# Optimization experiments

Measured on AMD Instinct MI355X. Metric: run time of the kernel, lower is better.

The kernel has to match this reference:

```python
import jax, jax.numpy as jnp
import numpy as np

DIM = 384
HEADS = 12
K = 3          # kernel_size
PAD = 1
STRIDE = 1
B, H, W = 8, 56, 56


def conv1x1(x, w, b=None):
    # x: [B,C,H,W], w: [O,C]
    y = jnp.einsum('bchw,oc->bohw', x, w)
    if b is not None:
        y = y + b[None, :, None, None]
    return y


def unfold(x, k, p, s):
    # torch nn.Unfold: returns patches [B, C, k*k, nH, nW], kernel row-major, channel-major overall
    Bx, C, Hx, Wx = x.shape
    nH = (Hx + 2 * p - k) // s + 1
    nW = (Wx + 2 * p - k) // s + 1
    xp = jnp.pad(x, ((0, 0), (0, 0), (p, p), (p, p)))
    cols = [xp[:, :, i:i + s * nH:s, j:j + s * nW:s] for i in range(k) for j in range(k)]
    return jnp.stack(cols, axis=2), nH, nW


def fold(col, Hx, Wx, k, p, s):
    # torch F.fold (col2im): scatter-add overlapping windows. col: [B, C, k*k, nH, nW]
    Bx, C, _, nH, nW = col.shape
    canvas = jnp.zeros((Bx, C, Hx + 2 * p, Wx + 2 * p), col.dtype)
    idx = 0
    for i in range(k):
        for j in range(k):
            canvas = canvas.at[:, :, i:i + s * nH:s, j:j + s * nW:s].add(col[:, :, idx])
            idx += 1
    return canvas[:, :, p:p + Hx, p:p + Wx]


def setup_inputs() -> dict:
    key = jax.random.key(0)
    ks = jax.random.split(key, 5)
    k2 = K * K
    x = jax.random.normal(ks[0], (B, DIM, H, W), dtype=jnp.float32)
    v_w = jax.random.normal(ks[1], (DIM, DIM), dtype=jnp.float32) * 0.02
    v_b = jnp.zeros((DIM,), dtype=jnp.float32)
    attn_w = jax.random.normal(ks[2], (k2 * k2 * HEADS, DIM), dtype=jnp.float32) * 0.02
    proj_w = jax.random.normal(ks[3], (DIM, DIM), dtype=jnp.float32) * 0.02
    return {'x': x, 'v_w': v_w, 'v_b': v_b, 'attn_w': attn_w, 'proj_w': proj_w}


def reference(x, v_w, v_b, attn_w, proj_w):
    Bx, C, Hx, Wx = x.shape
    k2 = K * K
    hd = C // HEADS  # head dim
    # value projection + unfold into overlapping k x k windows
    v = conv1x1(x, v_w, v_b)
    vcol, nH, nW = unfold(v, K, PAD, STRIDE)        # [B, C, k2, nH, nW]
    L = nH * nW
    v = vcol.reshape(Bx, HEADS, hd, k2, L)          # split C = (heads, hd), heads slow
    v = v.transpose(0, 1, 4, 3, 2)                  # [B, n, L, k2(d), hd]
    # adaptive avg pool to (nH, nW); with stride=1 this is identity (pool window 1)
    ph, pw = Hx // nH, Wx // nW
    xp = x.reshape(Bx, C, nH, ph, nW, pw).mean(axis=(3, 5))
    # per-pixel attention logits, channel layout = ((i*k2 + d)*HEADS + head)
    a = jnp.einsum('bchw,oc->bohw', xp, attn_w)     # [B, k2*k2*n, nH, nW]
    a = a.reshape(Bx, k2, k2, HEADS, L)             # [B, i, d, n, L]
    a = a.transpose(0, 3, 4, 1, 2)                  # [B, n, L, i, d]
    a = jax.nn.softmax(a, axis=-1)
    out = jnp.einsum('bnlid,bnldh->bnlih', a, v)    # [B, n, L, i, hd]
    out = out.transpose(0, 1, 4, 3, 2)              # [B, n, hd, i, L] -> channel (n*hd+h)
    out = out.reshape(Bx, C, k2, nH, nW)
    out = fold(out, Hx, Wx, K, PAD, STRIDE)         # scatter-add windows back
    return conv1x1(out, proj_w)
```

## Files before the change

### kernel.cpp

```cpp
#include <hip/hip_runtime.h>
#include <hip/hip_bf16.h>

#define DIM   384
#define HEADS 12
#define K2    9
#define HH    56
#define WW    56
#define HWP   3136
#define BB    8
#define AO    972
#define AOP   976
#define MCAT  1408
#define PP    3200
#define PPAD  3600
#define W60   60

#define WBLK     2688
#define HALOBLK  696

typedef __hip_bfloat16 bf16;
typedef short bf16x8 __attribute__((ext_vector_type(8)));
typedef short bf16x4v __attribute__((ext_vector_type(4)));
typedef float f32x4 __attribute__((ext_vector_type(4)));
typedef float f32x2 __attribute__((ext_vector_type(2)));

static __device__ __forceinline__ float b2f(bf16 v) { return __bfloat162float(v); }
static __device__ __forceinline__ float bs2f(short s) {
    return __uint_as_float(((unsigned int)(unsigned short)s) << 16);
}
static __device__ __forceinline__ short f2bs(float f) {
    __hip_bfloat16 h = __float2bfloat16(f);
    return *(short*)&h;
}
static __device__ __forceinline__ f32x2 unpk(unsigned int u) {
    f32x2 r;
    r[0] = __uint_as_float(u << 16);
    r[1] = __uint_as_float(u & 0xffff0000u);
    return r;
}

static __device__ __forceinline__ void gl_lds16(const bf16* g, bf16* l) {
    __builtin_amdgcn_global_load_lds(
        (const __attribute__((address_space(1))) unsigned int*)g,
        (__attribute__((address_space(3))) unsigned int*)l, 16, 0, 0);
}

__global__ __launch_bounds__(256) void prep_kernel(
        const float* __restrict__ x, const float* __restrict__ v_w,
        const float* __restrict__ attn_w, const float* __restrict__ proj_w,
        bf16* __restrict__ xT, bf16* __restrict__ wcat, bf16* __restrict__ wp,
        bf16* __restrict__ vP) {
    const int bid = blockIdx.x;
    if (bid < 400) {
        const int lane = threadIdx.x & 63, w = threadIdx.x >> 6;
        const int p = (bid % 50) * 64 + lane;
        const int b = bid / 50;
        bf16* dst = xT + ((size_t)b * PP + p) * DIM;
        if (p >= HWP) {
            bf16x8 z = {};
            for (int cg = w; cg < 48; cg += 4) *(bf16x8*)(dst + cg * 8) = z;
            return;
        }
        const float* src = x + (size_t)b * DIM * HWP + p;
        for (int cg = w; cg < 48; cg += 4) {
            bf16x8 v;
#pragma unroll
            for (int j = 0; j < 8; j++) v[j] = f2bs(src[(size_t)(cg * 8 + j) * HWP]);
            *(bf16x8*)(dst + cg * 8) = v;
        }
    } else if (bid < 400 + WBLK) {
        const int idx = (bid - 400) * 256 + threadIdx.x;
        const int NCAT = MCAT * DIM;
        if (idx < NCAT) {
            const int row = idx / DIM, col = idx % DIM;
            float v;
            if (row < 384) v = v_w[row * DIM + col];
            else { const int r2 = row - 384; v = (r2 < AO) ? attn_w[r2 * DIM + col] : 0.f; }
            *(short*)&wcat[idx] = f2bs(v);
        } else {
            const int j = idx - NCAT;
            if (j < 384 * DIM) *(short*)&wp[j] = f2bs(proj_w[j]);
        }
    } else {
        const int hidx = (bid - 400 - WBLK) * 256 + threadIdx.x;
        const int b = hidx / 22272;
        const int r = hidx % 22272;
        const int hp = r / 48, cgi = r % 48;
        int row, col;
        if (hp < 240) {
            const int rr = hp / 60;
            row = (rr < 2) ? rr : rr + 56;
            col = hp % 60;
        } else {
            const int h2 = hp - 240;
            row = 2 + (h2 >> 2);
            const int c4 = h2 & 3;
            col = (c4 < 2) ? c4 : c4 + 56;
        }
        bf16x8 z = {};
        *(bf16x8*)(vP + ((size_t)b * PPAD + row * W60 + col) * DIM + cgi * 8) = z;
    }
}

#define GEMM_MAIN_LOOP_V4(Ab, Bb, lA, lB, acc)                                 \
    for (int k0 = 0; k0 < DIM; k0 += 64) {                                     \
        _Pragma("unroll")                                                      \
        for (int r = 0; r < 4; r++) {                                          \
            int idx = r * 256 + t;                                             \
            int row = idx >> 3;                                                \
            int kq = ((idx & 7) - (row >> 1)) & 7;                             \
            gl_lds16(Ab + (size_t)row * DIM + k0 + kq * 8, lA + idx * 8);      \
        }                                                                      \
        _Pragma("unroll")                                                      \
        for (int r = 0; r < 4; r++) {                                          \
            int idx = r * 256 + t;                                             \
            int row = idx >> 3;                                                \
            int kq = ((idx & 7) - (row >> 1)) & 7;                             \
            gl_lds16(Bb + (size_t)row * DIM + k0 + kq * 8, lB + idx * 8);      \
        }                                                                      \
        __syncthreads();                                                       \
        _Pragma("unroll")                                                      \
        for (int h = 0; h < 2; h++) {                                          \
            const int swzh = (((h << 2) + quad + (l16 >> 1)) & 7) * 8;         \
            bf16x8 af[4], bfr[4];                                              \
            _Pragma("unroll")                                                  \
            for (int mt = 0; mt < 4; mt++)                                     \
                af[mt] = *(const bf16x8*)(lA + (wm * 64 + mt * 16 + l16) * 64 + swzh); \
            _Pragma("unroll")                                                  \
            for (int nt = 0; nt < 4; nt++)                                     \
                bfr[nt] = *(const bf16x8*)(lB + (wn * 64 + nt * 16 + l16) * 64 + swzh); \
            _Pragma("unroll")                                                  \
            for (int mt = 0; mt < 4; mt++)                                     \
                _Pragma("unroll")                                              \
                for (int nt = 0; nt < 4; nt++)                                 \
                    acc[mt][nt] = __builtin_amdgcn_mfma_f32_16x16x32_bf16(     \
                        af[mt], bfr[nt], acc[mt][nt], 0, 0, 0);                \
        }                                                                      \
        __syncthreads();                                                       \
    }

__global__ __launch_bounds__(256) void gemm12_kernel(
        const bf16* __restrict__ A, const bf16* __restrict__ Bt,
        const float* __restrict__ bias, bf16* __restrict__ vP,
        bf16* __restrict__ lT) {
    __shared__ bf16 lds[16384];
    bf16* lA = lds;
    bf16* lB = lds + 8192;
    const int t = threadIdx.x;
    const int lane = t & 63, w = t >> 6;
    const int wm = w & 1, wn = w >> 1;
    const int quad = lane >> 4, l16 = lane & 15;

    const int bid = blockIdx.x;
    const int swz = (bid & 7) * 275 + (bid >> 3);
    const int mtile = swz % 11;
    const int nb = swz / 11;
    const int ntile = nb % 25;
    const int b = nb / 25;
    const int n0 = ntile * 128;
    const int m0 = mtile * 128;

    const bf16* Ab = A + (size_t)m0 * DIM;
    const bf16* Bb = Bt + ((size_t)b * PP + n0) * DIM;

    f32x4 acc[4][4] = {};
    GEMM_MAIN_LOOP_V4(Ab, Bb, lA, lB, acc)

    const bool isv = (m0 < 384);
    const int ch0 = isv ? m0 : m0 - 384;

    bf16* wbuf = lds + w * 1152;
    const int nr = lane >> 2;
    const int mc = (lane & 3) * 16;
#pragma unroll
    for (int nt = 0; nt < 4; nt++) {
#pragma unroll
        for (int mt = 0; mt < 4; mt++) {
            float4 bi = make_float4(0.f, 0.f, 0.f, 0.f);
            if (isv) bi = *(const float4*)(bias + ch0 + wm * 64 + mt * 16 + quad * 4);
            bf16x4v pk;
            pk[0] = f2bs(acc[mt][nt][0] + bi.x);
            pk[1] = f2bs(acc[mt][nt][1] + bi.y);
            pk[2] = f2bs(acc[mt][nt][2] + bi.z);
            pk[3] = f2bs(acc[mt][nt][3] + bi.w);
            *(bf16x4v*)(wbuf + l16 * 72 + mt * 16 + quad * 4) = pk;
        }
        bf16x8 v0 = *(const bf16x8*)(wbuf + nr * 72 + mc);
        bf16x8 v1 = *(const bf16x8*)(wbuf + nr * 72 + mc + 8);
        const int p = n0 + wn * 64 + nt * 16 + nr;
        const int cc = ch0 + wm * 64 + mc;
        if (p < HWP && (isv || cc < AOP)) {
            bf16* dp;
            if (isv) {
                const int y = p / WW;
                dp = vP + ((size_t)b * PPAD + p + y * 4 + 122) * DIM + cc;
            } else {
                dp = lT + ((size_t)b * PP + p) * AOP + cc;
            }
            *(bf16x8*)dp = v0;
            *(bf16x8*)(dp + 8) = v1;
        }
    }
}

__global__ __launch_bounds__(256) void gemm_planar_kernel(
        const bf16* __restrict__ A, const bf16* __restrict__ Bt,
        float* __restrict__ out) {
    __shared__ bf16 lds[16384];
    bf16* lA = lds;
    bf16* lB = lds + 8192;
    const int t = threadIdx.x;
    const int lane = t & 63, w = t >> 6;
    const int wm = w & 1, wn = w >> 1;
    const int quad = lane >> 4, l16 = lane & 15;

    const int bid = blockIdx.x;
    const int swz = (bid & 7) * 75 + (bid >> 3);
    const int mtile = swz % 3;
    const int nb = swz / 3;
    const int ntile = nb % 25;
    const int b = nb / 25;
    const int n0 = ntile * 128;
    const int m0 = mtile * 128;

    const bf16* Ab = A + (size_t)m0 * DIM;
    const bf16* Bb = Bt + ((size_t)b * PP + n0) * DIM;

    f32x4 acc[4][4] = {};
    GEMM_MAIN_LOOP_V4(Ab, Bb, lA, lB, acc)

#pragma unroll
    for (int mt = 0; mt < 4; mt++) {
#pragma unroll
        for (int nt = 0; nt < 4; nt++) {
            int p = n0 + wn * 64 + nt * 16 + l16;
            if (p >= HWP) continue;
#pragma unroll
            for (int reg = 0; reg < 4; reg++) {
                int o = m0 + wm * 64 + mt * 16 + quad * 4 + reg;
                out[((size_t)b * DIM + o) * HWP + p] = acc[mt][nt][reg];
            }
        }
    }
}

__global__ __launch_bounds__(384) void attn_fold_kernel(
        const bf16* __restrict__ lT, const bf16* __restrict__ vP,
        bf16* __restrict__ cT) {
    __shared__ bf16 P[8 * 9 * 12 * 9];
    __shared__ float Wf[8 * 25 * 12];
    const int t = threadIdx.x;
    const int b = blockIdx.x & 7;
    const int pix0 = (blockIdx.x >> 3) * 8;
    const int Y = pix0 / WW, X0 = pix0 % WW;

    for (int r = t; r < 864; r += 384) {
        const int px = r / 108, rem = r % 108;
        const int i = rem / 12, n = rem % 12;
        const int ir = i / 3, ic = i % 3;
        const int yi = Y + 1 - ir, xi = X0 + px + 1 - ic;
        bf16* Pd = &P[r * 9];
        if (yi < 0 || yi >= HH || xi < 0 || xi >= WW) {
#pragma unroll
            for (int d = 0; d < K2; d++) *(short*)&Pd[d] = 0;
        } else {
            const bf16* base = lT + ((size_t)b * PP + yi * WW + xi) * AOP + i * 108 + n;
            float lv[K2];
            float m = -1e30f;
#pragma unroll
            for (int d = 0; d < K2; d++) {
                lv[d] = b2f(base[d * 12]);
                m = fmaxf(m, lv[d]);
            }
            float s = 0.f;
#pragma unroll
            for (int d = 0; d < K2; d++) { lv[d] = __expf(lv[d] - m); s += lv[d]; }
            const float inv = 1.f / s;
#pragma unroll
            for (int d = 0; d < K2; d++) *(short*)&Pd[d] = f2bs(lv[d] * inv);
        }
    }
    __syncthreads();

    if (t < 300) {
        const int off = t / 12, n = t % 12;
        const int dy = off / 5 - 2, dx = off % 5 - 2;
        const int ir_lo = max(0, -dy), ir_hi = min(2, 2 - dy);
        const int ic_lo = max(0, -dx), ic_hi = min(2, 2 - dx);
#pragma unroll
        for (int px = 0; px < 8; px++) {
            float wsum = 0.f;
            for (int ir = ir_lo; ir <= ir_hi; ir++)
                for (int ic = ic_lo; ic <= ic_hi; ic++) {
                    const int i = ir * 3 + ic;
                    const int d = (dy + ir) * 3 + (dx + ic);
                    wsum += b2f(P[((px * 9 + i) * 12 + n) * 9 + d]);
                }
            Wf[(px * 25 + off) * 12 + n] = wsum;
        }
    }
    __syncthreads();

    const int px = t / 48, cg = t % 48;
    const int X = X0 + px;
    const int n = cg >> 2;
    const float* Wp = &Wf[px * 300 + n];
    const bf16* vbp = vP + ((size_t)b * PPAD + (size_t)(Y + 2) * W60 + (X + 2)) * DIM + cg * 8;
    f32x2 a2[4] = {};
#pragma unroll
    for (int dy = -2; dy <= 2; dy++) {
        const bf16* rowb = vbp + dy * (W60 * DIM);
        const float* wrow = Wp + (dy + 2) * 60;
#pragma unroll
        for (int dx = -2; dx <= 2; dx++) {
            const float w = wrow[(dx + 2) * 12];
            const uint4 d = *(const uint4*)(rowb + dx * DIM);
            f32x2 w2; w2[0] = w; w2[1] = w;
            a2[0] = __builtin_elementwise_fma(unpk(d.x), w2, a2[0]);
            a2[1] = __builtin_elementwise_fma(unpk(d.y), w2, a2[1]);
            a2[2] = __builtin_elementwise_fma(unpk(d.z), w2, a2[2]);
            a2[3] = __builtin_elementwise_fma(unpk(d.w), w2, a2[3]);
        }
    }
    bf16x8 po;
#pragma unroll
    for (int j = 0; j < 4; j++) {
        po[2 * j]     = f2bs(a2[j][0]);
        po[2 * j + 1] = f2bs(a2[j][1]);
    }
    *(bf16x8*)(cT + ((size_t)b * PP + pix0 + px) * DIM + cg * 8) = po;
}

extern "C" void kernel_launch(void* const* d_in, const int* in_sizes, int n_in,
                              void* d_out, int out_size, void* d_ws, size_t ws_size,
                              hipStream_t stream) {
    const float* x      = (const float*)d_in[0];
    const float* v_w    = (const float*)d_in[1];
    const float* v_b    = (const float*)d_in[2];
    const float* attn_w = (const float*)d_in[3];
    const float* proj_w = (const float*)d_in[4];
    float* out = (float*)d_out;

    bf16* xT    = (bf16*)d_ws;
    bf16* vP    = xT + (size_t)BB * PP * DIM;
    bf16* lT    = vP + (size_t)BB * PPAD * DIM;
    bf16* wcat  = lT + (size_t)BB * PP * AOP;
    bf16* wp    = wcat + (size_t)MCAT * DIM;
    bf16* cT    = xT;

    const int nprep = 400 + WBLK + HALOBLK;
    prep_kernel<<<nprep, 256, 0, stream>>>(x, v_w, attn_w, proj_w, xT, wcat, wp, vP);

    gemm12_kernel<<<2200, 256, 0, stream>>>(wcat, xT, v_b, vP, lT);
    attn_fold_kernel<<<3136, 384, 0, stream>>>(lT, vP, cT);
    gemm_planar_kernel<<<600, 256, 0, stream>>>(wp, cT, out);
}
```

Baseline: 204.7 us.

## Double-buffer LDS in GEMM main loop and raise priority around MFMA compute

Splits the GEMM K-loop into separate stage and compute macros and uses two LDS buffers per operand. The next K-slice's global-to-LDS loads are issued before the MFMA work on the current slice, which halves the barriers per slice and overlaps load latency with compute. s_setprio is raised around the MFMA section. LDS use doubles to 64 KB per block, which may reduce how many blocks fit on a CU.

```diff
diff --git a/kernel.cpp b/kernel.cpp
--- a/kernel.cpp
+++ b/kernel.cpp
@@ -102,40 +102,56 @@
     }
 }
 
-#define GEMM_MAIN_LOOP_V4(Ab, Bb, lA, lB, acc)                                 \
-    for (int k0 = 0; k0 < DIM; k0 += 64) {                                     \
+#define GEMM_STAGE(Ab, Bb, lA, lB, koff)                                       \
+    {                                                                          \
         _Pragma("unroll")                                                      \
         for (int r = 0; r < 4; r++) {                                          \
             int idx = r * 256 + t;                                             \
             int row = idx >> 3;                                                \
             int kq = ((idx & 7) - (row >> 1)) & 7;                             \
-            gl_lds16(Ab + (size_t)row * DIM + k0 + kq * 8, lA + idx * 8);      \
+            gl_lds16(Ab + (size_t)row * DIM + (koff) + kq * 8, lA + idx * 8);  \
         }                                                                      \
         _Pragma("unroll")                                                      \
         for (int r = 0; r < 4; r++) {                                          \
             int idx = r * 256 + t;                                             \
             int row = idx >> 3;                                                \
             int kq = ((idx & 7) - (row >> 1)) & 7;                             \
-            gl_lds16(Bb + (size_t)row * DIM + k0 + kq * 8, lB + idx * 8);      \
+            gl_lds16(Bb + (size_t)row * DIM + (koff) + kq * 8, lB + idx * 8);  \
         }                                                                      \
-        __syncthreads();                                                       \
-        _Pragma("unroll")                                                      \
-        for (int h = 0; h < 2; h++) {                                          \
-            const int swzh = (((h << 2) + quad + (l16 >> 1)) & 7) * 8;         \
-            bf16x8 af[4], bfr[4];                                              \
-            _Pragma("unroll")                                                  \
-            for (int mt = 0; mt < 4; mt++)                                     \
-                af[mt] = *(const bf16x8*)(lA + (wm * 64 + mt * 16 + l16) * 64 + swzh); \
+    }
+
+#define GEMM_COMPUTE(lA, lB, acc)                                              \
+    __builtin_amdgcn_s_setprio(1);                                             \
+    _Pragma("unroll")                                                          \
+    for (int h = 0; h < 2; h++) {                                              \
+        const int swzh = (((h << 2) + quad + (l16 >> 1)) & 7) * 8;             \
+        bf16x8 af[4], bfr[4];                                                  \
+        _Pragma("unroll")                                                      \
+        for (int mt = 0; mt < 4; mt++)                                         \
+            af[mt] = *(const bf16x8*)((lA) + (wm * 64 + mt * 16 + l16) * 64 + swzh); \
+        _Pragma("unroll")                                                      \
+        for (int nt = 0; nt < 4; nt++)                                         \
+            bfr[nt] = *(const bf16x8*)((lB) + (wn * 64 + nt * 16 + l16) * 64 + swzh); \
+        _Pragma("unroll")                                                      \
+        for (int mt = 0; mt < 4; mt++)                                         \
             _Pragma("unroll")                                                  \
             for (int nt = 0; nt < 4; nt++)                                     \
-                bfr[nt] = *(const bf16x8*)(lB + (wn * 64 + nt * 16 + l16) * 64 + swzh); \
-            _Pragma("unroll")                                                  \
-            for (int mt = 0; mt < 4; mt++)                                     \
-                _Pragma("unroll")                                              \
-                for (int nt = 0; nt < 4; nt++)                                 \
-                    acc[mt][nt] = __builtin_amdgcn_mfma_f32_16x16x32_bf16(     \
-                        af[mt], bfr[nt], acc[mt][nt], 0, 0, 0);                \
-        }                                                                      \
+                acc[mt][nt] = __builtin_amdgcn_mfma_f32_16x16x32_bf16(         \
+                    af[mt], bfr[nt], acc[mt][nt], 0, 0, 0);                    \
+    }                                                                          \
+    __builtin_amdgcn_s_setprio(0);
+
+#define GEMM_MAIN_LOOP_V5(Ab, Bb, acc)                                         \
+    GEMM_STAGE(Ab, Bb, lA0, lB0, 0)                                            \
+    __syncthreads();                                                           \
+    _Pragma("unroll")                                                          \
+    for (int k2i = 0; k2i < 3; k2i++) {                                        \
+        const int kbase = k2i * 128;                                           \
+        GEMM_STAGE(Ab, Bb, lA1, lB1, kbase + 64)                               \
+        GEMM_COMPUTE(lA0, lB0, acc)                                            \
+        __syncthreads();                                                       \
+        if (kbase + 128 < DIM) GEMM_STAGE(Ab, Bb, lA0, lB0, kbase + 128)       \
+        GEMM_COMPUTE(lA1, lB1, acc)                                            \
         __syncthreads();                                                       \
     }
 
@@ -143,9 +159,11 @@
         const bf16* __restrict__ A, const bf16* __restrict__ Bt,
         const float* __restrict__ bias, bf16* __restrict__ vP,
         bf16* __restrict__ lT) {
-    __shared__ bf16 lds[16384];
-    bf16* lA = lds;
-    bf16* lB = lds + 8192;
+    __shared__ bf16 lds[32768];
+    bf16* lA0 = lds;
+    bf16* lB0 = lds + 8192;
+    bf16* lA1 = lds + 16384;
+    bf16* lB1 = lds + 24576;
     const int t = threadIdx.x;
     const int lane = t & 63, w = t >> 6;
     const int wm = w & 1, wn = w >> 1;
@@ -164,7 +182,7 @@
     const bf16* Bb = Bt + ((size_t)b * PP + n0) * DIM;
 
     f32x4 acc[4][4] = {};
-    GEMM_MAIN_LOOP_V4(Ab, Bb, lA, lB, acc)
+    GEMM_MAIN_LOOP_V5(Ab, Bb, acc)
 
     const bool isv = (m0 < 384);
     const int ch0 = isv ? m0 : m0 - 384;
@@ -206,9 +224,11 @@
 __global__ __launch_bounds__(256) void gemm_planar_kernel(
         const bf16* __restrict__ A, const bf16* __restrict__ Bt,
         float* __restrict__ out) {
-    __shared__ bf16 lds[16384];
-    bf16* lA = lds;
-    bf16* lB = lds + 8192;
+    __shared__ bf16 lds[32768];
+    bf16* lA0 = lds;
+    bf16* lB0 = lds + 8192;
+    bf16* lA1 = lds + 16384;
+    bf16* lB1 = lds + 24576;
     const int t = threadIdx.x;
     const int lane = t & 63, w = t >> 6;
     const int wm = w & 1, wn = w >> 1;
@@ -227,7 +247,7 @@
     const bf16* Bb = Bt + ((size_t)b * PP + n0) * DIM;
 
     f32x4 acc[4][4] = {};
-    GEMM_MAIN_LOOP_V4(Ab, Bb, lA, lB, acc)
+    GEMM_MAIN_LOOP_V5(Ab, Bb, acc)
 
 #pragma unroll
     for (int mt = 0; mt < 4; mt++) {
```

After: 207.0 us. No clear change (+1.1%).
